# Performance work log

Measured on AMD Instinct MI355X. Metric: run time of the kernel, lower is better.

The kernel has to match this reference:

```python
import jax, jax.numpy as jnp
import numpy as np

TEMPERATURE = 1.0
NEG = -1e30  # finite 'masked' logit: exp underflows to 0, no NaN in grads


def setup_inputs() -> dict:
    key = jax.random.key(0)
    k1, k2, k3 = jax.random.split(key, 3)
    B, L = 8192, 4096
    predictions = jax.random.normal(k1, (B, L), dtype=jnp.float32)
    targets = jax.random.normal(k2, (B, L), dtype=jnp.float32)
    nan_mask = jax.random.uniform(k3, (B, L)) < 0.2
    targets = jnp.where(nan_mask, jnp.nan, targets)
    return {"predictions": predictions, "targets": targets}


def reference(predictions, targets):
    # valid entries = non-NaN targets; rows need >1 valid entry to contribute
    mask = ~jnp.isnan(targets)                          # [B, L] bool
    valid_rows = jnp.sum(mask, axis=-1) > 1             # [B]

    p_logits = jnp.where(mask, predictions, NEG) / TEMPERATURE
    t_logits = jnp.where(mask, targets, NEG) / TEMPERATURE  # where() also kills NaNs

    log_p = jax.nn.log_softmax(p_logits, axis=-1)       # [B, L]
    log_q = jax.nn.log_softmax(t_logits, axis=-1)
    q = jnp.exp(log_q)

    # per-row KL(q || p) summed over valid entries (masked softmax already gives
    # q ~ 0 at invalid slots; where() guards against 0 * inf)
    kl_row = jnp.sum(jnp.where(mask, q * (log_q - log_p), 0.0), axis=-1)  # [B]

    n_valid = jnp.sum(valid_rows)
    total = jnp.sum(jnp.where(valid_rows, kl_row, 0.0))
    return jnp.where(n_valid > 0, total / jnp.maximum(n_valid, 1), 0.0)
```

## Files before the change

### kernel.cpp

```cpp
#include <hip/hip_runtime.h>

#define NEGV  -1e30f
#define NSLOT 64

__device__ __forceinline__ float wave_reduce_sum(float v) {
    #pragma unroll
    for (int off = 32; off > 0; off >>= 1)
        v += __shfl_xor(v, off);
    return v;
}

struct __align__(64) Slot {
    unsigned long long kl;
    unsigned           cnt;
    unsigned           pad[13];
};

__global__ __launch_bounds__(256) void listnet_row_kernel(
    const float* __restrict__ preds,
    const float* __restrict__ targs,
    Slot* __restrict__ slots)
{
    const int wid  = threadIdx.x >> 6;
    const int lane = threadIdx.x & 63;
    const int row  = blockIdx.x * 4 + wid;

    const float4* __restrict__ p4 =
        reinterpret_cast<const float4*>(preds) + (size_t)row * 1024;
    const float4* __restrict__ t4 =
        reinterpret_cast<const float4*>(targs) + (size_t)row * 1024;

    float s_t = 0.f, s_p = 0.f, A = 0.f, cnt = 0.f;

    #pragma unroll
    for (int c = 0; c < 16; ++c) {
        float4 tv = t4[c * 64 + lane];
        float4 pv = p4[c * 64 + lane];
        const float tarr[4] = {tv.x, tv.y, tv.z, tv.w};
        const float parr[4] = {pv.x, pv.y, pv.z, pv.w};
        #pragma unroll
        for (int j = 0; j < 4; ++j) {
            float t = tarr[j];
            bool  valid = (t == t);
            float tc = valid ? t       : NEGV;
            float pc = valid ? parr[j] : NEGV;
            float et = __expf(tc);
            float ep = __expf(pc);
            s_t += et;
            s_p += ep;
            A    = fmaf(et, tc - pc, A);
            cnt += valid ? 1.f : 0.f;
        }
    }

    s_t = wave_reduce_sum(s_t);
    s_p = wave_reduce_sum(s_p);
    A   = wave_reduce_sum(A);
    cnt = wave_reduce_sum(cnt);

    if (lane == 0 && cnt > 1.5f) {
        float kl = A / s_t + __logf(s_p / s_t);
        long long q = llrintf(kl * 4294967296.f);
        Slot* s = &slots[blockIdx.x & (NSLOT - 1)];
        atomicAdd(&s->kl, (unsigned long long)q);
        atomicAdd(&s->cnt, 1u);
    }
}

__global__ void listnet_finish_kernel(
    const Slot* __restrict__ slots,
    float* __restrict__ out)
{
    const int lane = threadIdx.x & 63;
    unsigned long long q = 0ull;
    unsigned           n = 0u;
    if (lane < NSLOT) {
        q = slots[lane].kl;
        n = slots[lane].cnt;
    }
    #pragma unroll
    for (int off = 32; off > 0; off >>= 1) {
        q += __shfl_xor((unsigned long long)q, off);
        n += __shfl_xor(n, off);
    }
    if (lane == 0) {
        double kl = (double)(long long)q * (1.0 / 4294967296.0);
        out[0] = (n > 0u) ? (float)(kl / (double)n) : 0.f;
    }
}

extern "C" void kernel_launch(void* const* d_in, const int* in_sizes, int n_in,
                              void* d_out, int out_size, void* d_ws, size_t ws_size,
                              hipStream_t stream) {
    const float* preds = (const float*)d_in[0];
    const float* targs = (const float*)d_in[1];
    const int L = 4096;
    const int B = in_sizes[0] / L;

    Slot* slots = (Slot*)d_ws;

    hipMemsetAsync(slots, 0, NSLOT * sizeof(Slot), stream);
    listnet_row_kernel<<<B / 4, 256, 0, stream>>>(preds, targs, slots);
    listnet_finish_kernel<<<1, 64, 0, stream>>>(slots, (float*)d_out);
}
```

Measured before the change: 51.19 us.

## Process each row cooperatively across the whole block with shared-memory reduction

```diff
diff --git a/kernel.cpp b/kernel.cpp
--- a/kernel.cpp
+++ b/kernel.cpp
@@ -1,6 +1,7 @@
 #include <hip/hip_runtime.h>
 
 #define NEGV  -1e30f
+#define ROWS  4
 #define NSLOT 64
 
 __device__ __forceinline__ float wave_reduce_sum(float v) {
@@ -21,49 +22,80 @@
     const float* __restrict__ targs,
     Slot* __restrict__ slots)
 {
-    const int wid  = threadIdx.x >> 6;
-    const int lane = threadIdx.x & 63;
-    const int row  = blockIdx.x * 4 + wid;
+    const int tid  = threadIdx.x;
+    const int wid  = tid >> 6;
+    const int lane = tid & 63;
+    const int row0 = blockIdx.x * ROWS;
 
-    const float4* __restrict__ p4 =
-        reinterpret_cast<const float4*>(preds) + (size_t)row * 1024;
-    const float4* __restrict__ t4 =
-        reinterpret_cast<const float4*>(targs) + (size_t)row * 1024;
-
-    float s_t = 0.f, s_p = 0.f, A = 0.f, cnt = 0.f;
+    __shared__ float sm[ROWS][4][4];
 
     #pragma unroll
-    for (int c = 0; c < 16; ++c) {
-        float4 tv = t4[c * 64 + lane];
-        float4 pv = p4[c * 64 + lane];
-        const float tarr[4] = {tv.x, tv.y, tv.z, tv.w};
-        const float parr[4] = {pv.x, pv.y, pv.z, pv.w};
+    for (int r = 0; r < ROWS; ++r) {
+        const float4* __restrict__ p4 =
+            reinterpret_cast<const float4*>(preds) + (size_t)(row0 + r) * 1024;
+        const float4* __restrict__ t4 =
+            reinterpret_cast<const float4*>(targs) + (size_t)(row0 + r) * 1024;
+
+        float4 t0 = t4[tid      ], t1 = t4[tid + 256],
+               t2 = t4[tid + 512], t3 = t4[tid + 768];
+        float4 p0 = p4[tid      ], p1 = p4[tid + 256],
+               p2 = p4[tid + 512], p3 = p4[tid + 768];
+        __builtin_amdgcn_sched_barrier(0);
+
+        const float4 tv[4] = {t0, t1, t2, t3};
+        const float4 pv[4] = {p0, p1, p2, p3};
+
+        float s_t = 0.f, s_p = 0.f, A = 0.f, cnt = 0.f;
         #pragma unroll
-        for (int j = 0; j < 4; ++j) {
-            float t = tarr[j];
-            bool  valid = (t == t);
-            float tc = valid ? t       : NEGV;
-            float pc = valid ? parr[j] : NEGV;
-            float et = __expf(tc);
-            float ep = __expf(pc);
-            s_t += et;
-            s_p += ep;
-            A    = fmaf(et, tc - pc, A);
-            cnt += valid ? 1.f : 0.f;
+        for (int i = 0; i < 4; ++i) {
+            const float tarr[4] = {tv[i].x, tv[i].y, tv[i].z, tv[i].w};
+            const float parr[4] = {pv[i].x, pv[i].y, pv[i].z, pv[i].w};
+            #pragma unroll
+            for (int j = 0; j < 4; ++j) {
+                float t = tarr[j];
+                bool  valid = (t == t);
+                float tc = valid ? t       : NEGV;
+                float pc = valid ? parr[j] : NEGV;
+                float et = __expf(tc);
+                float ep = __expf(pc);
+                s_t += et;
+                s_p += ep;
+                A    = fmaf(et, tc - pc, A);
+                cnt += valid ? 1.f : 0.f;
+            }
+        }
+
+        s_t = wave_reduce_sum(s_t);
+        s_p = wave_reduce_sum(s_p);
+        A   = wave_reduce_sum(A);
+        cnt = wave_reduce_sum(cnt);
+        if (lane == 0) {
+            sm[r][0][wid] = s_t; sm[r][1][wid] = s_p;
+            sm[r][2][wid] = A;   sm[r][3][wid] = cnt;
         }
     }
+    __syncthreads();
 
-    s_t = wave_reduce_sum(s_t);
-    s_p = wave_reduce_sum(s_p);
-    A   = wave_reduce_sum(A);
-    cnt = wave_reduce_sum(cnt);
-
-    if (lane == 0 && cnt > 1.5f) {
-        float kl = A / s_t + __logf(s_p / s_t);
-        long long q = llrintf(kl * 4294967296.f);
-        Slot* s = &slots[blockIdx.x & (NSLOT - 1)];
-        atomicAdd(&s->kl, (unsigned long long)q);
-        atomicAdd(&s->cnt, 1u);
+    if (wid == 0) {
+        float kl = 0.f, fl = 0.f;
+        if (lane < ROWS) {
+            float st = sm[lane][0][0] + sm[lane][0][1] + sm[lane][0][2] + sm[lane][0][3];
+            float sp = sm[lane][1][0] + sm[lane][1][1] + sm[lane][1][2] + sm[lane][1][3];
+            float Aa = sm[lane][2][0] + sm[lane][2][1] + sm[lane][2][2] + sm[lane][2][3];
+            float cn = sm[lane][3][0] + sm[lane][3][1] + sm[lane][3][2] + sm[lane][3][3];
+            if (cn > 1.5f) {
+                kl = Aa / st + __logf(sp / st);
+                fl = 1.f;
+            }
+        }
+        kl += __shfl_xor(kl, 1); fl += __shfl_xor(fl, 1);
+        kl += __shfl_xor(kl, 2); fl += __shfl_xor(fl, 2);
+        if (lane == 0 && fl > 0.f) {
+            long long q = llrintf(kl * 4294967296.f);
+            Slot* s = &slots[blockIdx.x & (NSLOT - 1)];
+            atomicAdd(&s->kl, (unsigned long long)q);
+            atomicAdd(&s->cnt, (unsigned)fl);
+        }
     }
 }
 
@@ -94,12 +126,13 @@
                               hipStream_t stream) {
     const float* preds = (const float*)d_in[0];
     const float* targs = (const float*)d_in[1];
-    const int L = 4096;
-    const int B = in_sizes[0] / L;
+    const int L  = 4096;
+    const int B  = in_sizes[0] / L;
+    const int NB = B / ROWS;
 
     Slot* slots = (Slot*)d_ws;
 
     hipMemsetAsync(slots, 0, NSLOT * sizeof(Slot), stream);
-    listnet_row_kernel<<<B / 4, 256, 0, stream>>>(preds, targs, slots);
+    listnet_row_kernel<<<NB, 256, 0, stream>>>(preds, targs, slots);
     listnet_finish_kernel<<<1, 64, 0, stream>>>(slots, (float*)d_out);
 }
```

Result: no change. 50.95 us (-0.5%).
